# Kernel tuning notes

Hardware: AMD Instinct MI355X
Metric: run time of the kernel (lower is better)

## Reference

```python
import jax, jax.numpy as jnp
import numpy as np
import math

B, C, N = 8, 512, 2048

def setup_inputs() -> dict:
    key = jax.random.key(0)
    ks = jax.random.split(key, 7)
    s = 0.02
    return {
        "x": jax.random.normal(ks[0], (B, C, N), dtype=jnp.float32),
        "Wq": jax.random.normal(ks[1], (C // 2, C), dtype=jnp.float32) * s,
        "bq": jax.random.normal(ks[2], (C // 2,), dtype=jnp.float32) * s,
        "Wk": jax.random.normal(ks[3], (C // 2, C), dtype=jnp.float32) * s,
        "bk": jax.random.normal(ks[4], (C // 2,), dtype=jnp.float32) * s,
        "Wv": jax.random.normal(ks[5], (C, C), dtype=jnp.float32) * s,
        "bv": jax.random.normal(ks[6], (C,), dtype=jnp.float32) * s,
    }

def reference(x, Wq, bq, Wk, bk, Wv, bv):
    # pointwise conv1d == channel matmul: (O,C) x (B,C,N) -> (B,O,N)
    Q = jnp.einsum('oc,bcn->bon', Wq, x) + bq[None, :, None]  # (B, C/2, N)
    K = jnp.einsum('oc,bcn->bon', Wk, x) + bk[None, :, None]  # (B, C/2, N)
    V = jnp.einsum('oc,bcn->bon', Wv, x) + bv[None, :, None]  # (B, C, N)
    scale = 1.0 / math.sqrt(K.shape[1])
    A = jnp.einsum('bcn,bcm->bnm', Q, K) * scale              # (B, N, N)
    A = jax.nn.softmax(A, axis=-1)
    out = jnp.einsum('bcm,bnm->bcn', V, A)                    # V @ A^T
    return x + out
```

## Files before the change

### kernel.cpp

```cpp
#include <hip/hip_runtime.h>

#define B_ 8
#define C_ 512
#define N_ 2048
#define O_ 256

typedef unsigned short u16;
typedef unsigned char u8;
typedef unsigned int uint;
typedef float f32x4 __attribute__((ext_vector_type(4)));
typedef int i32x8 __attribute__((ext_vector_type(8)));

#define AS1 __attribute__((address_space(1)))
#define AS3 __attribute__((address_space(3)))

__device__ __forceinline__ u16 f2bf(float f) {
  union { float f; unsigned u; } v; v.f = f;
  return (u16)((v.u + 0x7fffu + ((v.u >> 16) & 1u)) >> 16);
}
__device__ __forceinline__ float bf2f(u16 h) {
  union { uint u; float f; } v; v.u = ((uint)h) << 16; return v.f;
}
__device__ __forceinline__ uint pk4_e4m3(float a, float b, float c, float d) {
  int r = __builtin_amdgcn_cvt_pk_fp8_f32(a, b, 0, false);
  r = __builtin_amdgcn_cvt_pk_fp8_f32(c, d, r, true);
  return (uint)r;
}

union MxFrag { i32x8 v; uint4 q[2]; };

template<int AR>
__device__ __forceinline__ void mx_stage_tile(
    const u8* __restrict__ Ag, int lda,
    const u8* __restrict__ Bg, int ldb, int k0,
    u8 (&As)[AR][128], u8 (&Bs)[128][128], int w, int r8, int gsrc)
{
#pragma unroll
  for (int s = 0; s < AR / 32; s++) {
    int row = (w * (AR / 32) + s) * 8;
    __builtin_amdgcn_global_load_lds(
        (const AS1 uint*)(Ag + (size_t)(row + r8) * lda + k0 + gsrc * 16),
        (AS3 uint*)(&As[row][0]), 16, 0, 0);
  }
#pragma unroll
  for (int s = 0; s < 4; s++) {
    int row = (w * 4 + s) * 8;
    __builtin_amdgcn_global_load_lds(
        (const AS1 uint*)(Bg + (size_t)(row + r8) * ldb + k0 + gsrc * 16),
        (AS3 uint*)(&Bs[row][0]), 16, 0, 0);
  }
}

template<int MI, int AR>
__device__ __forceinline__ void mx_compute_tile(
    const u8 (&As)[AR][128], const u8 (&Bs)[128][128],
    f32x4 (&acc)[MI][4], int wm, int wn, int lrow, int quad)
{
  const int swz = lrow & 7;
  const int g0 = (quad * 2) ^ swz, g1 = (quad * 2 + 1) ^ swz;
  MxFrag af[MI], bfr[4];
#pragma unroll
  for (int i = 0; i < MI; i++) {
    const u8* rp = &As[wm + i * 16 + lrow][0];
    af[i].q[0] = *(const uint4*)(rp + g0 * 16);
    af[i].q[1] = *(const uint4*)(rp + g1 * 16);
  }
#pragma unroll
  for (int j = 0; j < 4; j++) {
    const u8* rp = &Bs[wn + j * 16 + lrow][0];
    bfr[j].q[0] = *(const uint4*)(rp + g0 * 16);
    bfr[j].q[1] = *(const uint4*)(rp + g1 * 16);
  }
  asm volatile("s_waitcnt lgkmcnt(0)" ::: "memory");
#pragma unroll
  for (int i = 0; i < MI; i++)
#pragma unroll
    for (int j = 0; j < 4; j++)
      acc[i][j] = __builtin_amdgcn_mfma_scale_f32_16x16x128_f8f6f4(
          af[i].v, bfr[j].v, acc[i][j],
          0, 0,
          0, 0x7f7f7f7f,
          0, 0x7f7f7f7f);
}

template<int NT, int AR, int MI>
__device__ __forceinline__ void mx_mainloop_db(
    const u8* __restrict__ Ag, int lda,
    const u8* __restrict__ Bg, int ldb,
    u8 (&As)[2][AR][128], u8 (&Bs)[2][128][128],
    f32x4 (&acc)[MI][4], int wm, int wn)
{
  const int t = threadIdx.x;
  const int lane = t & 63;
  const int w = t >> 6;
  const int lrow = lane & 15, quad = lane >> 4;
  const int r8 = lane >> 3;
  const int gsrc = (lane & 7) ^ r8;
  constexpr int LPT = AR / 32 + 4;

  mx_stage_tile<AR>(Ag, lda, Bg, ldb, 0, As[0], Bs[0], w, r8, gsrc);
  if (NT > 1)
    mx_stage_tile<AR>(Ag, lda, Bg, ldb, 128, As[1], Bs[1], w, r8, gsrc);

#pragma unroll
  for (int tt = 0; tt < NT; ++tt) {
    if (tt + 1 < NT)
      asm volatile("s_waitcnt vmcnt(%0)" :: "n"(LPT) : "memory");
    else
      asm volatile("s_waitcnt vmcnt(0)" ::: "memory");
    __builtin_amdgcn_s_barrier();
    mx_compute_tile<MI, AR>(As[tt & 1], Bs[tt & 1], acc, wm, wn, lrow, quad);
    __builtin_amdgcn_s_barrier();
    if (tt + 2 < NT)
      mx_stage_tile<AR>(Ag, lda, Bg, ldb, (tt + 2) * 128,
                        As[tt & 1], Bs[tt & 1], w, r8, gsrc);
  }
}

__global__ __launch_bounds__(256) void prep_kernel(
    const float* __restrict__ x,
    const float* __restrict__ Wq, const float* __restrict__ Wk,
    const float* __restrict__ Wv,
    u8* __restrict__ xT8, u8* __restrict__ Wq8, u8* __restrict__ Wk8,
    u8* __restrict__ Wv8, float* __restrict__ rowsum)
{
  __shared__ u16 tile[64][72];
  const int bid = blockIdx.x;
  const int t = threadIdx.x;
  if (bid < 2048) {
    int b = bid >> 8;
    int n0 = (bid & 31) * 64;
    int c0 = ((bid >> 5) & 7) * 64;
    const float* src = x + (size_t)b * C_ * N_ + (size_t)c0 * N_ + n0;
    int r = t >> 4;
    int f4 = (t & 15) * 4;
#pragma unroll
    for (int i = 0; i < 4; i++) {
      int c = r + 16 * i;
      float4 v = *(const float4*)(src + (size_t)c * N_ + f4);
      tile[f4 + 0][c] = f2bf(v.x);
      tile[f4 + 1][c] = f2bf(v.y);
      tile[f4 + 2][c] = f2bf(v.z);
      tile[f4 + 3][c] = f2bf(v.w);
    }
    __syncthreads();
    u8* dst = xT8 + (size_t)b * N_ * C_ + (size_t)n0 * C_ + c0;
    int n = t >> 2;
    int cc = (t & 3) * 16;
    uint4 d;
    d.x = pk4_e4m3(bf2f(tile[n][cc + 0]), bf2f(tile[n][cc + 1]),
                   bf2f(tile[n][cc + 2]), bf2f(tile[n][cc + 3]));
    d.y = pk4_e4m3(bf2f(tile[n][cc + 4]), bf2f(tile[n][cc + 5]),
                   bf2f(tile[n][cc + 6]), bf2f(tile[n][cc + 7]));
    d.z = pk4_e4m3(bf2f(tile[n][cc + 8]), bf2f(tile[n][cc + 9]),
                   bf2f(tile[n][cc + 10]), bf2f(tile[n][cc + 11]));
    d.w = pk4_e4m3(bf2f(tile[n][cc + 12]), bf2f(tile[n][cc + 13]),
                   bf2f(tile[n][cc + 14]), bf2f(tile[n][cc + 15]));
    *(uint4*)(dst + (size_t)n * C_ + cc) = d;
  } else {
    int gid = (bid - 2048) * 256 + t;
    const float* src; u8* dst; int o;
    if (gid < 32768)      { src = Wq; dst = Wq8; o = gid; }
    else if (gid < 65536) { src = Wk; dst = Wk8; o = gid - 32768; }
    else                  { src = Wv; dst = Wv8; o = gid - 65536; }
    float4 v = *(const float4*)(src + (size_t)o * 4);
    *(uint*)(dst + (size_t)o * 4) = pk4_e4m3(v.x, v.y, v.z, v.w);
    if (gid < 4096) {
      float4 z = {0.f, 0.f, 0.f, 0.f};
      *(float4*)(rowsum + gid * 4) = z;
    }
  }
}

__global__ __launch_bounds__(256) void proj_all_kernel(
    const u8* __restrict__ xT8,
    const u8* __restrict__ Wq8, const float* __restrict__ bq,
    const u8* __restrict__ Wk8, const float* __restrict__ bk,
    const u8* __restrict__ Wv8, const float* __restrict__ bv,
    u8* __restrict__ Qt8, u8* __restrict__ Kt8, u8* __restrict__ V8)
{
  __shared__ __align__(16) u8 As[2][128][128], Bs[2][128][128];
  const int n0 = blockIdx.x * 128;
  const int b = blockIdx.y;
  const int sub = blockIdx.z;
  const u8* xTb = xT8 + (size_t)b * N_ * C_ + (size_t)n0 * C_;

  const f32x4 zero = {0.f, 0.f, 0.f, 0.f};
  f32x4 acc[4][4];
#pragma unroll
  for (int i = 0; i < 4; i++)
#pragma unroll
    for (int j = 0; j < 4; j++) acc[i][j] = zero;

  const int lane = threadIdx.x & 63;
  const int w = threadIdx.x >> 6;
  const int wm = (w >> 1) * 64, wn = (w & 1) * 64;
  const int quad = lane >> 4, lcol = lane & 15;

  if (sub < 4) {
    const int isK = sub >> 1;
    const int o0 = (sub & 1) * 128;
    const u8* Wg = (isK ? Wk8 : Wq8) + (size_t)o0 * C_;
    const float* bias = isK ? bk : bq;
    u8* outp = (isK ? Kt8 : Qt8) + (size_t)b * N_ * O_;

    mx_mainloop_db<4, 128, 4>(Wg, C_, xTb, C_, As, Bs, acc, wm, wn);

#pragma unroll
    for (int i = 0; i < 4; i++) {
      int obase = o0 + wm + i * 16 + quad * 4;
      float4 bb = *(const float4*)(bias + obase);
#pragma unroll
      for (int j = 0; j < 4; j++) {
        int n = n0 + wn + j * 16 + lcol;
        uint d = pk4_e4m3(acc[i][j][0] + bb.x, acc[i][j][1] + bb.y,
                          acc[i][j][2] + bb.z, acc[i][j][3] + bb.w);
        *(uint*)(outp + (size_t)n * O_ + obase) = d;
      }
    }
  } else {
    const int c0 = (sub - 4) * 128;
    const u8* Wg = Wv8 + (size_t)c0 * C_;
    u8* outp = V8 + (size_t)b * C_ * N_;

    mx_mainloop_db<4, 128, 4>(xTb, C_, Wg, C_, As, Bs, acc, wm, wn);

#pragma unroll
    for (int j = 0; j < 4; j++) {
      int c = c0 + wn + j * 16 + lcol;
      float bb = bv[c];
#pragma unroll
      for (int i = 0; i < 4; i++) {
        int nbase = n0 + wm + i * 16 + quad * 4;
        uint d = pk4_e4m3(acc[i][j][0] + bb, acc[i][j][1] + bb,
                          acc[i][j][2] + bb, acc[i][j][3] + bb);
        *(uint*)(outp + (size_t)c * N_ + nbase) = d;
      }
    }
  }
}

__global__ __launch_bounds__(256) void attn_s_kernel(
    const u8* __restrict__ Qt8, const u8* __restrict__ Kt8,
    u8* __restrict__ P, float* __restrict__ rowsum)
{
  __shared__ __align__(16) u8 As[2][128][128], Bs[2][128][128];
  int b = blockIdx.z;
  int m0 = blockIdx.x * 128, n0 = blockIdx.y * 128;
  const u8* Ag = Kt8 + (size_t)b * N_ * O_ + (size_t)m0 * O_;
  const u8* Bg = Qt8 + (size_t)b * N_ * O_ + (size_t)n0 * O_;

  const f32x4 zero = {0.f, 0.f, 0.f, 0.f};
  f32x4 acc[4][4];
#pragma unroll
  for (int i = 0; i < 4; i++)
#pragma unroll
    for (int j = 0; j < 4; j++) acc[i][j] = zero;

  const int lane = threadIdx.x & 63;
  const int w = threadIdx.x >> 6;
  const int wm = (w >> 1) * 64, wn = (w & 1) * 64;
  const int quad = lane >> 4, lcol = lane & 15;

  mx_mainloop_db<2, 128, 4>(Ag, O_, Bg, O_, As, Bs, acc, wm, wn);

  u8* Pp = P + (size_t)b * N_ * N_;
  float* rs = rowsum + (size_t)b * N_;

  float partial[4];
#pragma unroll
  for (int j = 0; j < 4; j++) partial[j] = 0.f;

#pragma unroll
  for (int j = 0; j < 4; j++) {
    int n = n0 + wn + j * 16 + lcol;
#pragma unroll
    for (int i = 0; i < 4; i++) {
      int mbase = m0 + wm + i * 16 + quad * 4;
      float p0 = __expf(acc[i][j][0] * 0.0625f);
      float p1 = __expf(acc[i][j][1] * 0.0625f);
      float p2 = __expf(acc[i][j][2] * 0.0625f);
      float p3 = __expf(acc[i][j][3] * 0.0625f);
      *(uint*)(Pp + (size_t)n * N_ + mbase) = pk4_e4m3(p0, p1, p2, p3);
      partial[j] += p0 + p1 + p2 + p3;
    }
  }
#pragma unroll
  for (int msk = 16; msk < 64; msk <<= 1)
#pragma unroll
    for (int j = 0; j < 4; j++)
      partial[j] += __shfl_xor(partial[j], msk);
  if (quad == 0) {
#pragma unroll
    for (int j = 0; j < 4; j++)
      atomicAdd(&rs[n0 + wn + j * 16 + lcol], partial[j]);
  }
}

__global__ __launch_bounds__(256) void attn_o_kernel(
    const u8* __restrict__ V, const u8* __restrict__ P,
    const float* __restrict__ rowsum, const float* __restrict__ x,
    float* __restrict__ out)
{
  __shared__ __align__(16) u8 As[2][64][128], Bs[2][128][128];
  const int b = blockIdx.z;
  const int c0 = blockIdx.y * 64, n0 = blockIdx.x * 128;
  const u8* Ag = V + (size_t)b * C_ * N_ + (size_t)c0 * N_;
  const u8* Bg = P + (size_t)b * N_ * N_ + (size_t)n0 * N_;

  const int t = threadIdx.x;
  const int lane = t & 63;
  const int w = t >> 6;
  const int wm = (w >> 1) * 32;
  const int wn = (w & 1) * 64;
  const int lrow = lane & 15, quad = lane >> 4;

  const f32x4 zero = {0.f, 0.f, 0.f, 0.f};
  f32x4 acc[2][4];
#pragma unroll
  for (int i = 0; i < 2; i++)
#pragma unroll
    for (int j = 0; j < 4; j++) acc[i][j] = zero;

  mx_mainloop_db<16, 64, 2>(Ag, N_, Bg, N_, As, Bs, acc, wm, wn);

  const float* xb = x + (size_t)b * C_ * N_;
  float* ob = out + (size_t)b * C_ * N_;
  float invl[4];
#pragma unroll
  for (int j = 0; j < 4; j++)
    invl[j] = 1.f / rowsum[b * N_ + n0 + wn + j * 16 + lrow];

#pragma unroll
  for (int i = 0; i < 2; i++)
#pragma unroll
    for (int rr = 0; rr < 4; rr++) {
      int c = c0 + wm + i * 16 + quad * 4 + rr;
#pragma unroll
      for (int j = 0; j < 4; j++) {
        int n = n0 + wn + j * 16 + lrow;
        size_t idx = (size_t)c * N_ + n;
        ob[idx] = xb[idx] + acc[i][j][rr] * invl[j];
      }
    }
}

extern "C" void kernel_launch(void* const* d_in, const int* in_sizes, int n_in,
                              void* d_out, int out_size, void* d_ws, size_t ws_size,
                              hipStream_t stream)
{
  (void)in_sizes; (void)n_in; (void)out_size; (void)ws_size;
  const float* x  = (const float*)d_in[0];
  const float* Wq = (const float*)d_in[1];
  const float* bq = (const float*)d_in[2];
  const float* Wk = (const float*)d_in[3];
  const float* bk = (const float*)d_in[4];
  const float* Wv = (const float*)d_in[5];
  const float* bv = (const float*)d_in[6];
  float* out = (float*)d_out;

  char* ws = (char*)d_ws;
  size_t off = 0;
  auto carve = [&](size_t bytes) -> char* {
    char* p = ws + off;
    off += (bytes + 255) & ~(size_t)255;
    return p;
  };
  u8*  xT8  = (u8*) carve((size_t)B_ * N_ * C_);
  u8*  Wq8  = (u8*) carve((size_t)O_ * C_);
  u8*  Wk8  = (u8*) carve((size_t)O_ * C_);
  u8*  Wv8  = (u8*) carve((size_t)C_ * C_);
  u8*  Qt8  = (u8*) carve((size_t)B_ * N_ * O_);
  u8*  Kt8  = (u8*) carve((size_t)B_ * N_ * O_);
  u8*  Vb   = (u8*) carve((size_t)B_ * C_ * N_);
  u8*  P    = (u8*) carve((size_t)B_ * N_ * N_);
  float* rowsum = (float*)carve((size_t)B_ * N_ * 4);

  prep_kernel<<<dim3(2560), 256, 0, stream>>>(
      x, Wq, Wk, Wv, xT8, Wq8, Wk8, Wv8, rowsum);
  proj_all_kernel<<<dim3(N_ / 128, B_, 8), 256, 0, stream>>>(
      xT8, Wq8, bq, Wk8, bk, Wv8, bv, Qt8, Kt8, Vb);
  attn_s_kernel<<<dim3(N_ / 128, N_ / 128, B_), 256, 0, stream>>>(Qt8, Kt8, P, rowsum);
  attn_o_kernel<<<dim3(N_ / 128, C_ / 64, B_), 256, 0, stream>>>(Vb, P, rowsum, x, out);
}
```

Baseline: 177.5 us.

## Fuse score, softmax and PV into a flash-style attention kernel

```diff
diff --git a/kernel.cpp b/kernel.cpp
--- a/kernel.cpp
+++ b/kernel.cpp
@@ -29,6 +29,26 @@
 
 union MxFrag { i32x8 v; uint4 q[2]; };
 
+__device__ __forceinline__ f32x4 mxmfma(const MxFrag& a, const MxFrag& b,
+                                        f32x4 c) {
+  return __builtin_amdgcn_mfma_scale_f32_16x16x128_f8f6f4(
+      a.v, b.v, c,
+      0, 0,
+      0, 0x7f7f7f7f,
+      0, 0x7f7f7f7f);
+}
+
+template<int R>
+__device__ __forceinline__ MxFrag readFrag(const u8 (&S)[R][128], int row,
+                                           int quad, int swz) {
+  MxFrag f;
+  const u8* rp = &S[row][0];
+  const int g0 = (quad * 2) ^ swz, g1 = (quad * 2 + 1) ^ swz;
+  f.q[0] = *(const uint4*)(rp + g0 * 16);
+  f.q[1] = *(const uint4*)(rp + g1 * 16);
+  return f;
+}
+
 template<int AR>
 __device__ __forceinline__ void mx_stage_tile(
     const u8* __restrict__ Ag, int lda,
@@ -57,30 +77,19 @@
     f32x4 (&acc)[MI][4], int wm, int wn, int lrow, int quad)
 {
   const int swz = lrow & 7;
-  const int g0 = (quad * 2) ^ swz, g1 = (quad * 2 + 1) ^ swz;
   MxFrag af[MI], bfr[4];
 #pragma unroll
-  for (int i = 0; i < MI; i++) {
-    const u8* rp = &As[wm + i * 16 + lrow][0];
-    af[i].q[0] = *(const uint4*)(rp + g0 * 16);
-    af[i].q[1] = *(const uint4*)(rp + g1 * 16);
-  }
-#pragma unroll
-  for (int j = 0; j < 4; j++) {
-    const u8* rp = &Bs[wn + j * 16 + lrow][0];
-    bfr[j].q[0] = *(const uint4*)(rp + g0 * 16);
-    bfr[j].q[1] = *(const uint4*)(rp + g1 * 16);
-  }
+  for (int i = 0; i < MI; i++)
+    af[i] = readFrag(As, wm + i * 16 + lrow, quad, swz);
+#pragma unroll
+  for (int j = 0; j < 4; j++)
+    bfr[j] = readFrag(Bs, wn + j * 16 + lrow, quad, swz);
   asm volatile("s_waitcnt lgkmcnt(0)" ::: "memory");
 #pragma unroll
   for (int i = 0; i < MI; i++)
 #pragma unroll
     for (int j = 0; j < 4; j++)
-      acc[i][j] = __builtin_amdgcn_mfma_scale_f32_16x16x128_f8f6f4(
-          af[i].v, bfr[j].v, acc[i][j],
-          0, 0,
-          0, 0x7f7f7f7f,
-          0, 0x7f7f7f7f);
+      acc[i][j] = mxmfma(af[i], bfr[j], acc[i][j]);
 }
 
 template<int NT, int AR, int MI>
@@ -122,7 +131,7 @@
     const float* __restrict__ Wq, const float* __restrict__ Wk,
     const float* __restrict__ Wv,
     u8* __restrict__ xT8, u8* __restrict__ Wq8, u8* __restrict__ Wk8,
-    u8* __restrict__ Wv8, float* __restrict__ rowsum)
+    u8* __restrict__ Wv8)
 {
   __shared__ u16 tile[64][72];
   const int bid = blockIdx.x;
@@ -165,10 +174,6 @@
     else                  { src = Wv; dst = Wv8; o = gid - 65536; }
     float4 v = *(const float4*)(src + (size_t)o * 4);
     *(uint*)(dst + (size_t)o * 4) = pk4_e4m3(v.x, v.y, v.z, v.w);
-    if (gid < 4096) {
-      float4 z = {0.f, 0.f, 0.f, 0.f};
-      *(float4*)(rowsum + gid * 4) = z;
-    }
   }
 }
 
@@ -240,107 +245,175 @@
   }
 }
 
-__global__ __launch_bounds__(256) void attn_s_kernel(
+__global__ __launch_bounds__(512, 2) void attn_fused_kernel(
     const u8* __restrict__ Qt8, const u8* __restrict__ Kt8,
-    u8* __restrict__ P, float* __restrict__ rowsum)
-{
-  __shared__ __align__(16) u8 As[2][128][128], Bs[2][128][128];
-  int b = blockIdx.z;
-  int m0 = blockIdx.x * 128, n0 = blockIdx.y * 128;
-  const u8* Ag = Kt8 + (size_t)b * N_ * O_ + (size_t)m0 * O_;
-  const u8* Bg = Qt8 + (size_t)b * N_ * O_ + (size_t)n0 * O_;
-
-  const f32x4 zero = {0.f, 0.f, 0.f, 0.f};
-  f32x4 acc[4][4];
-#pragma unroll
-  for (int i = 0; i < 4; i++)
-#pragma unroll
-    for (int j = 0; j < 4; j++) acc[i][j] = zero;
-
-  const int lane = threadIdx.x & 63;
-  const int w = threadIdx.x >> 6;
-  const int wm = (w >> 1) * 64, wn = (w & 1) * 64;
-  const int quad = lane >> 4, lcol = lane & 15;
-
-  mx_mainloop_db<2, 128, 4>(Ag, O_, Bg, O_, As, Bs, acc, wm, wn);
-
-  u8* Pp = P + (size_t)b * N_ * N_;
-  float* rs = rowsum + (size_t)b * N_;
-
-  float partial[4];
-#pragma unroll
-  for (int j = 0; j < 4; j++) partial[j] = 0.f;
-
-#pragma unroll
-  for (int j = 0; j < 4; j++) {
-    int n = n0 + wn + j * 16 + lcol;
-#pragma unroll
-    for (int i = 0; i < 4; i++) {
-      int mbase = m0 + wm + i * 16 + quad * 4;
-      float p0 = __expf(acc[i][j][0] * 0.0625f);
-      float p1 = __expf(acc[i][j][1] * 0.0625f);
-      float p2 = __expf(acc[i][j][2] * 0.0625f);
-      float p3 = __expf(acc[i][j][3] * 0.0625f);
-      *(uint*)(Pp + (size_t)n * N_ + mbase) = pk4_e4m3(p0, p1, p2, p3);
-      partial[j] += p0 + p1 + p2 + p3;
-    }
-  }
-#pragma unroll
-  for (int msk = 16; msk < 64; msk <<= 1)
-#pragma unroll
-    for (int j = 0; j < 4; j++)
-      partial[j] += __shfl_xor(partial[j], msk);
-  if (quad == 0) {
-#pragma unroll
-    for (int j = 0; j < 4; j++)
-      atomicAdd(&rs[n0 + wn + j * 16 + lcol], partial[j]);
-  }
-}
-
-__global__ __launch_bounds__(256) void attn_o_kernel(
-    const u8* __restrict__ V, const u8* __restrict__ P,
-    const float* __restrict__ rowsum, const float* __restrict__ x,
+    const u8* __restrict__ V8, const float* __restrict__ x,
     float* __restrict__ out)
 {
-  __shared__ __align__(16) u8 As[2][64][128], Bs[2][128][128];
-  const int b = blockIdx.z;
-  const int c0 = blockIdx.y * 64, n0 = blockIdx.x * 128;
-  const u8* Ag = V + (size_t)b * C_ * N_ + (size_t)c0 * N_;
-  const u8* Bg = P + (size_t)b * N_ * N_ + (size_t)n0 * N_;
+  __shared__ __align__(16) u8 Qs[2][128][128];
+  __shared__ __align__(16) u8 Ks[2][128][128];
+  __shared__ __align__(16) u8 Vs[256][128];
+  __shared__ __align__(16) u8 Ps[128][128];
+  __shared__ float rsum2[4][128];
+
+  const int L = blockIdx.x + (int)(blockIdx.y * gridDim.x) +
+                (int)(blockIdx.z * gridDim.x * gridDim.y);
+  const int b = L & 7;
+  const int c0 = ((L >> 3) & 1) * 256;
+  const int n0 = (L >> 4) * 128;
+
+  const u8* Qb = Qt8 + (size_t)b * N_ * O_ + (size_t)n0 * O_;
+  const u8* Kb = Kt8 + (size_t)b * N_ * O_;
+  const u8* Vg = V8 + (size_t)b * C_ * N_ + (size_t)c0 * N_;
 
   const int t = threadIdx.x;
   const int lane = t & 63;
   const int w = t >> 6;
-  const int wm = (w >> 1) * 32;
-  const int wn = (w & 1) * 64;
   const int lrow = lane & 15, quad = lane >> 4;
+  const int swz = lrow & 7;
+  const int r8 = lane >> 3;
+  const int gsrc = (lane & 7) ^ r8;
+  const int wm_s = (w & 3) * 32;
+  const int wn   = (w >> 2) * 64;
+  const int wm_o = (w & 3) * 64;
+
+  auto stageQ = [&]() {
+#pragma unroll
+    for (int s = 0; s < 4; s++) {
+      int idx = w * 4 + s;
+      int ch = idx >> 4, row = (idx & 15) * 8;
+      __builtin_amdgcn_global_load_lds(
+          (const AS1 uint*)(Qb + (size_t)(row + r8) * O_ + ch * 128 + gsrc * 16),
+          (AS3 uint*)(&Qs[ch][row][0]), 16, 0, 0);
+    }
+  };
+  auto stageK = [&](int m0) {
+#pragma unroll
+    for (int s = 0; s < 4; s++) {
+      int idx = w * 4 + s;
+      int ch = idx >> 4, row = (idx & 15) * 8;
+      __builtin_amdgcn_global_load_lds(
+          (const AS1 uint*)(Kb + (size_t)(m0 + row + r8) * O_ + ch * 128 + gsrc * 16),
+          (AS3 uint*)(&Ks[ch][row][0]), 16, 0, 0);
+    }
+  };
+  auto stageV = [&](int m0) {
+#pragma unroll
+    for (int s = 0; s < 4; s++) {
+      int idx = w * 4 + s;
+      int row = idx * 8;
+      __builtin_amdgcn_global_load_lds(
+          (const AS1 uint*)(Vg + (size_t)(row + r8) * N_ + m0 + gsrc * 16),
+          (AS3 uint*)(&Vs[row][0]), 16, 0, 0);
+    }
+  };
+
+  stageQ();
+  stageK(0);
+  stageV(0);
+  asm volatile("s_waitcnt vmcnt(8)" ::: "memory");
+  __builtin_amdgcn_s_barrier();
+
+  MxFrag qf[2][4];
+#pragma unroll
+  for (int ch = 0; ch < 2; ch++)
+#pragma unroll
+    for (int j = 0; j < 4; j++)
+      qf[ch][j] = readFrag(Qs[ch], wn + j * 16 + lrow, quad, swz);
 
   const f32x4 zero = {0.f, 0.f, 0.f, 0.f};
-  f32x4 acc[2][4];
-#pragma unroll
-  for (int i = 0; i < 2; i++)
-#pragma unroll
-    for (int j = 0; j < 4; j++) acc[i][j] = zero;
-
-  mx_mainloop_db<16, 64, 2>(Ag, N_, Bg, N_, As, Bs, acc, wm, wn);
-
+  f32x4 acco[4][4];
+#pragma unroll
+  for (int i = 0; i < 4; i++)
+#pragma unroll
+    for (int j = 0; j < 4; j++) acco[i][j] = zero;
+  float partial[4] = {0.f, 0.f, 0.f, 0.f};
+
+#pragma unroll 1
+  for (int mt = 0; mt < 16; ++mt) {
+    asm volatile("s_waitcnt vmcnt(4)" ::: "memory");
+    __builtin_amdgcn_s_barrier();
+
+    f32x4 accs[2][4];
+#pragma unroll
+    for (int i = 0; i < 2; i++)
+#pragma unroll
+      for (int j = 0; j < 4; j++) accs[i][j] = zero;
+#pragma unroll
+    for (int ch = 0; ch < 2; ch++) {
+      MxFrag a0 = readFrag(Ks[ch], wm_s + lrow, quad, swz);
+      MxFrag a1 = readFrag(Ks[ch], wm_s + 16 + lrow, quad, swz);
+#pragma unroll
+      for (int j = 0; j < 4; j++) {
+        accs[0][j] = mxmfma(a0, qf[ch][j], accs[0][j]);
+        accs[1][j] = mxmfma(a1, qf[ch][j], accs[1][j]);
+      }
+    }
+#pragma unroll
+    for (int i = 0; i < 2; i++) {
+      const int mb = wm_s + i * 16 + quad * 4;
+      const int gw = mb >> 4;
+#pragma unroll
+      for (int j = 0; j < 4; j++) {
+        const int n = wn + j * 16 + lrow;
+        float p0 = __expf(accs[i][j][0] * 0.0625f);
+        float p1 = __expf(accs[i][j][1] * 0.0625f);
+        float p2 = __expf(accs[i][j][2] * 0.0625f);
+        float p3 = __expf(accs[i][j][3] * 0.0625f);
+        partial[j] += (p0 + p1) + (p2 + p3);
+        *(uint*)(&Ps[n][((gw ^ (n & 7)) << 4) | (quad * 4)]) =
+            pk4_e4m3(p0, p1, p2, p3);
+      }
+    }
+    asm volatile("s_waitcnt lgkmcnt(0) vmcnt(0)" ::: "memory");
+    __builtin_amdgcn_s_barrier();
+    if (mt + 1 < 16) stageK((mt + 1) * 128);
+
+    MxFrag vf[4], pf[4];
+#pragma unroll
+    for (int i = 0; i < 4; i++)
+      vf[i] = readFrag(Vs, wm_o + i * 16 + lrow, quad, swz);
+#pragma unroll
+    for (int j = 0; j < 4; j++)
+      pf[j] = readFrag(Ps, wn + j * 16 + lrow, quad, swz);
+#pragma unroll
+    for (int i = 0; i < 4; i++)
+#pragma unroll
+      for (int j = 0; j < 4; j++)
+        acco[i][j] = mxmfma(vf[i], pf[j], acco[i][j]);
+    asm volatile("s_waitcnt lgkmcnt(0)" ::: "memory");
+    __builtin_amdgcn_s_barrier();
+    if (mt + 1 < 16) stageV((mt + 1) * 128);
+  }
+
+#pragma unroll
+  for (int msk = 16; msk < 64; msk <<= 1)
+#pragma unroll
+    for (int j = 0; j < 4; j++) partial[j] += __shfl_xor(partial[j], msk);
+  if (quad == 0)
+#pragma unroll
+    for (int j = 0; j < 4; j++)
+      rsum2[w & 3][wn + j * 16 + lrow] = partial[j];
+  __syncthreads();
+
+  float invl[4];
+#pragma unroll
+  for (int j = 0; j < 4; j++) {
+    const int n = wn + j * 16 + lrow;
+    invl[j] = 1.f / (rsum2[0][n] + rsum2[1][n] + rsum2[2][n] + rsum2[3][n]);
+  }
   const float* xb = x + (size_t)b * C_ * N_;
   float* ob = out + (size_t)b * C_ * N_;
-  float invl[4];
-#pragma unroll
-  for (int j = 0; j < 4; j++)
-    invl[j] = 1.f / rowsum[b * N_ + n0 + wn + j * 16 + lrow];
-
-#pragma unroll
-  for (int i = 0; i < 2; i++)
+#pragma unroll
+  for (int i = 0; i < 4; i++)
 #pragma unroll
     for (int rr = 0; rr < 4; rr++) {
-      int c = c0 + wm + i * 16 + quad * 4 + rr;
+      const int cg = c0 + wm_o + i * 16 + quad * 4 + rr;
 #pragma unroll
       for (int j = 0; j < 4; j++) {
-        int n = n0 + wn + j * 16 + lrow;
-        size_t idx = (size_t)c * N_ + n;
-        ob[idx] = xb[idx] + acc[i][j][rr] * invl[j];
+        const int ng = n0 + wn + j * 16 + lrow;
+        const size_t idx = (size_t)cg * N_ + ng;
+        ob[idx] = xb[idx] + acco[i][j][rr] * invl[j];
       }
     }
 }
@@ -373,13 +446,11 @@
   u8*  Qt8  = (u8*) carve((size_t)B_ * N_ * O_);
   u8*  Kt8  = (u8*) carve((size_t)B_ * N_ * O_);
   u8*  Vb   = (u8*) carve((size_t)B_ * C_ * N_);
-  u8*  P    = (u8*) carve((size_t)B_ * N_ * N_);
-  float* rowsum = (float*)carve((size_t)B_ * N_ * 4);
 
   prep_kernel<<<dim3(2560), 256, 0, stream>>>(
-      x, Wq, Wk, Wv, xT8, Wq8, Wk8, Wv8, rowsum);
+      x, Wq, Wk, Wv, xT8, Wq8, Wk8, Wv8);
   proj_all_kernel<<<dim3(N_ / 128, B_, 8), 256, 0, stream>>>(
       xT8, Wq8, bq, Wk8, bk, Wv8, bv, Qt8, Kt8, Vb);
-  attn_s_kernel<<<dim3(N_ / 128, N_ / 128, B_), 256, 0, stream>>>(Qt8, Kt8, P, rowsum);
-  attn_o_kernel<<<dim3(N_ / 128, C_ / 64, B_), 256, 0, stream>>>(Vb, P, rowsum, x, out);
-}
+  attn_fused_kernel<<<dim3(N_ / 128, 2, B_), 512, 0, stream>>>(
+      Qt8, Kt8, Vb, x, out);
+}
```

Result: no change. 175.9 us (-0.9%).
